# Kernel optimization log

Hardware: AMD Instinct MI355X
Metric: run time of the kernel (lower is better)

## Reference

```python
import jax, jax.numpy as jnp
import numpy as np

N = 131072          # batch of (action, condition) pairs
ACT_D = 12          # action_dim
COND_D = 256        # condition_dim
K = 256             # num_embeddings (codebook size)
E = 16              # embedding_dim
H1, H2 = 512, 256   # encoder_hidden_dims
COMMIT = 0.25       # commitment_cost
EPS_NORM = 1e-12    # F.normalize eps


def _normalize(x):
    n = jnp.linalg.norm(x, axis=-1, keepdims=True)
    return x / jnp.maximum(n, EPS_NORM)


def setup_inputs() -> dict:
    key = jax.random.key(0)
    ks = jax.random.split(key, 16)
    s = 0.02
    return {
        "actions": jax.random.normal(ks[0], (N, ACT_D), jnp.float32),
        "conditions": jax.random.normal(ks[1], (N, COND_D), jnp.float32),
        # encoder: (COND_D+ACT_D) -> H1 -> H2 -> E  (weights stored [in, out])
        "enc_w1": jax.random.normal(ks[2], (COND_D + ACT_D, H1), jnp.float32) * s,
        "enc_b1": jnp.zeros((H1,), jnp.float32),
        "enc_w2": jax.random.normal(ks[3], (H1, H2), jnp.float32) * s,
        "enc_b2": jnp.zeros((H2,), jnp.float32),
        "enc_w3": jax.random.normal(ks[4], (H2, E), jnp.float32) * s,
        "enc_b3": jnp.zeros((E,), jnp.float32),
        # decoder: (COND_D+E) -> H2 -> H1 -> ACT_D
        "dec_w1": jax.random.normal(ks[5], (COND_D + E, H2), jnp.float32) * s,
        "dec_b1": jnp.zeros((H2,), jnp.float32),
        "dec_w2": jax.random.normal(ks[6], (H2, H1), jnp.float32) * s,
        "dec_b2": jnp.zeros((H1,), jnp.float32),
        "dec_w3": jax.random.normal(ks[7], (H1, ACT_D), jnp.float32) * s,
        "dec_b3": jnp.zeros((ACT_D,), jnp.float32),
        # codebook, init U(-1/K, 1/K) like nn.Embedding in the module
        "embedding": jax.random.uniform(ks[8], (K, E), jnp.float32, -1.0 / K, 1.0 / K),
    }


def reference(actions, conditions, enc_w1, enc_b1, enc_w2, enc_b2, enc_w3, enc_b3,
              dec_w1, dec_b1, dec_w2, dec_b2, dec_w3, dec_b3, embedding):
    sg = jax.lax.stop_gradient
    elu = jax.nn.elu

    # ---- encoder ----
    x = jnp.concatenate([actions, conditions], axis=-1)          # [N, ACT_D+COND_D]
    h = elu(x @ enc_w1 + enc_b1)
    h = elu(h @ enc_w2 + enc_b2)
    z = h @ enc_w3 + enc_b3                                      # [N, E]

    # ---- vector quantizer (distance='cos') ----
    normed_in = sg(_normalize(z))                                # inputs.detach()
    normed_w = _normalize(embedding)
    distances = normed_in @ normed_w.T                           # [N, K] cosine sims

    idx = jnp.argmax(distances, axis=-1)                         # [N]
    quantized = embedding[idx]                                   # one-hot @ codebook == gather

    e_latent_loss = COMMIT * jnp.mean((sg(quantized) - z) ** 2)
    q_latent_loss = jnp.mean((quantized - sg(z)) ** 2)
    quantized_st = z + sg(quantized - z)                         # straight-through

    counts = jnp.zeros((K,), distances.dtype).at[idx].add(1.0)
    avg_probs = counts / N                                       # mean of one-hot encodings
    perplexity = jnp.exp(-jnp.sum(avg_probs * jnp.log(avg_probs + 1e-10)))

    # ---- contrastive loss (training branch, deterministic part) ----
    sortd = jnp.sort(distances, axis=0)                          # ascending per codeword
    n_pos = max(1, N // K)
    dis_pos = jnp.mean(sortd[-n_pos:, :], axis=0, keepdims=True) # [1, K] hardest positives
    dis_neg = sortd[: N // 2, :]                                 # [N//2, K]
    dis = jnp.concatenate([dis_pos, dis_neg], axis=0).T / 0.07   # [K, 1+N//2]
    # cross-entropy with target class 0
    contra_loss = jnp.mean(jax.nn.logsumexp(dis, axis=1) - dis[:, 0])

    # ---- decoder ----
    d = jnp.concatenate([quantized_st, conditions], axis=-1)     # [N, E+COND_D]
    d = elu(d @ dec_w1 + dec_b1)
    d = elu(d @ dec_w2 + dec_b2)
    reconstructed = d @ dec_w3 + dec_b3                          # [N, ACT_D]

    reconstruction_loss = jnp.mean((reconstructed - actions) ** 2)

    return (reconstructed, quantized_st, idx.astype(jnp.int32), q_latent_loss,
            e_latent_loss, contra_loss, perplexity, reconstruction_loss)
```

## Files before the change

kernel.cpp:

```cpp
#include <hip/hip_runtime.h>
#include <hip/hip_bf16.h>
#include <math.h>

#define NROWS 131072
#define ACT_D 12
#define COND_D 256
#define KEMB 256
#define EDIM 16
#define H1D 512
#define H2D 256
#define NB 16384

typedef __attribute__((ext_vector_type(8))) _Float16 half8;
typedef __attribute__((ext_vector_type(4))) float floatx4;
typedef unsigned short ushort_t;

#define LO_SCALE 4096.0f
#define INV_LO_SCALE 2.44140625e-4f


__global__ void init_kernel(int* counts, float* outScal) {
    int t = threadIdx.x;
    counts[t] = 0;
    if (t < 5) outScal[t] = 0.0f;
}

__device__ inline ushort_t f16bits(_Float16 h) { return __builtin_bit_cast(ushort_t, h); }
__device__ inline float f16pair(ushort_t a, ushort_t b) {
    return (float)__builtin_bit_cast(_Float16, a)
         + (float)__builtin_bit_cast(_Float16, b) * INV_LO_SCALE;
}
__device__ inline void splitf(float v, ushort_t& hi, ushort_t& lo) {
    _Float16 h = (_Float16)v;
    _Float16 l = (_Float16)((v - (float)h) * LO_SCALE);
    hi = f16bits(h); lo = f16bits(l);
}

__device__ inline void gload_lds16(const void* g, void* lds) {
    __builtin_amdgcn_global_load_lds((const __attribute__((address_space(1))) void*)g,
                                     (__attribute__((address_space(3))) void*)lds, 16, 0, 0);
}

__global__ __launch_bounds__(256)
void convw_kernel(const float* __restrict__ W, ushort_t* __restrict__ Whi,
                  ushort_t* __restrict__ Wlo, int K, int N, int Kp)
{
    int n = blockIdx.x;
    int k = blockIdx.y * 256 + threadIdx.x;
    if (k >= Kp) return;
    float v = (k < K) ? W[(long)k * N + n] : 0.0f;
    ushort_t h, l; splitf(v, h, l);
    Whi[(long)n * Kp + k] = h;
    Wlo[(long)n * Kp + k] = l;
}

template<int CONCAT>
__global__ __launch_bounds__(256, 3)
void gemm_f16x3_kernel(const void* A0v, const void* A1v,
                       const ushort_t* __restrict__ Bhi, const ushort_t* __restrict__ Blo,
                       const float* __restrict__ bias,
                       ushort_t* __restrict__ Chi, ushort_t* __restrict__ Clo,
                       int Nw, int Kp, int Kvalid)
{
    __shared__ uint lds[4096];
    const int tid = threadIdx.x;
    const int w = tid >> 6, l = tid & 63;
    const int quad = l >> 4, lr = l & 15;
    const long rowBase = (long)blockIdx.x * 64;
    const int colBase = blockIdx.y * 128;
    const int nQ = w * 32;

    floatx4 accH[4][2], accX[4][2];
#pragma unroll
    for (int i = 0; i < 4; ++i)
#pragma unroll
        for (int j = 0; j < 2; ++j) { accH[i][j] = (floatx4)(0.0f); accX[i][j] = (floatx4)(0.0f); }

    const long nIdx0 = colBase + nQ + lr;
    const ushort_t* pF0h = Bhi + nIdx0 * Kp + quad * 8;
    const ushort_t* pF1h = pF0h + 16 * Kp;
    const ushort_t* pF0l = Blo + nIdx0 * Kp + quad * 8;
    const ushort_t* pF1l = pF0l + 16 * Kp;

    uint4 bch0, bch1, bcl0, bcl1;
    uint4 bnh0, bnh1, bnl0, bnl1;
    auto loadBcur = [&](int k0) {
        bch0 = *(const uint4*)(pF0h + k0);
        bch1 = *(const uint4*)(pF1h + k0);
        bcl0 = *(const uint4*)(pF0l + k0);
        bcl1 = *(const uint4*)(pF1l + k0);
    };
    auto loadBnext = [&](int k0) {
        bnh0 = *(const uint4*)(pF0h + k0);
        bnh1 = *(const uint4*)(pF1h + k0);
        bnl0 = *(const uint4*)(pF0l + k0);
        bnl1 = *(const uint4*)(pF1l + k0);
    };
    auto promoteB = [&]() {
        bch0 = bnh0; bch1 = bnh1; bcl0 = bnl0; bcl1 = bnl1;
    };

    const ushort_t* pAh = (const ushort_t*)A0v + (rowBase + l) * Kp + w * 8;
    const ushort_t* pAl = (const ushort_t*)A1v + (rowBase + l) * Kp + w * 8;
    auto stageA0 = [&](int buf, int k0) {
        uint* d = &lds[buf * 2048 + w * 256];
        gload_lds16(pAh + k0, d);
        gload_lds16(pAl + k0, d + 1024);
    };

    const float* A1p = (const float*)A0v;
    const float* A2p = (const float*)A1v;
    const long grow = rowBase + l;

    auto aload = [&](float* v, int k0) {
        const int kk = k0 + w * 8;
        if (kk >= CONCAT && kk + 8 <= Kvalid) {
            const float* p = A2p + grow * COND_D + (kk - CONCAT);
            *(float4*)&v[0] = *(const float4*)p;
            *(float4*)&v[4] = *(const float4*)(p + 4);
        } else if (kk + 8 <= CONCAT) {
            const float* p = A1p + grow * CONCAT + kk;
            *(float4*)&v[0] = *(const float4*)p;
            *(float4*)&v[4] = *(const float4*)(p + 4);
        } else {
#pragma unroll
            for (int i = 0; i < 8; ++i) {
                int k = kk + i;
                v[i] = (k < CONCAT) ? A1p[grow * CONCAT + k]
                     : (k < Kvalid) ? A2p[grow * COND_D + (k - CONCAT)] : 0.0f;
            }
        }
    };
    auto awrite = [&](int buf, const float* v) {
        uint hh[4], ll[4];
#pragma unroll
        for (int i = 0; i < 4; ++i) {
            ushort_t h0, l0, h1, l1;
            splitf(v[2 * i], h0, l0);
            splitf(v[2 * i + 1], h1, l1);
            hh[i] = (uint)h0 | ((uint)h1 << 16);
            ll[i] = (uint)l0 | ((uint)l1 << 16);
        }
        *(uint4*)&lds[buf * 2048 + w * 256 + l * 4]        = *(uint4*)hh;
        *(uint4*)&lds[buf * 2048 + 1024 + w * 256 + l * 4] = *(uint4*)ll;
    };

    auto compute = [&](int buf) {
        const int base = buf * 2048;
        half8 bh0 = __builtin_bit_cast(half8, bch0);
        half8 bh1 = __builtin_bit_cast(half8, bch1);
        half8 bl0 = __builtin_bit_cast(half8, bcl0);
        half8 bl1 = __builtin_bit_cast(half8, bcl1);
#pragma unroll
        for (int im = 0; im < 4; ++im) {
            int aoff = base + quad * 256 + (im * 16 + lr) * 4;
            half8 ah = __builtin_bit_cast(half8, *(uint4*)&lds[aoff]);
            half8 al = __builtin_bit_cast(half8, *(uint4*)&lds[aoff + 1024]);
            accH[im][0] = __builtin_amdgcn_mfma_f32_16x16x32_f16(ah, bh0, accH[im][0], 0, 0, 0);
            accX[im][0] = __builtin_amdgcn_mfma_f32_16x16x32_f16(ah, bl0, accX[im][0], 0, 0, 0);
            accX[im][0] = __builtin_amdgcn_mfma_f32_16x16x32_f16(al, bh0, accX[im][0], 0, 0, 0);
            accH[im][1] = __builtin_amdgcn_mfma_f32_16x16x32_f16(ah, bh1, accH[im][1], 0, 0, 0);
            accX[im][1] = __builtin_amdgcn_mfma_f32_16x16x32_f16(ah, bl1, accX[im][1], 0, 0, 0);
            accX[im][1] = __builtin_amdgcn_mfma_f32_16x16x32_f16(al, bh1, accX[im][1], 0, 0, 0);
        }
    };

    const int kTiles = Kp / 32;
    int cur = 0;
    float v[8];

    if constexpr (CONCAT == 0) {
        stageA0(0, 0);
        loadBcur(0);
        __syncthreads();
    } else {
        aload(v, 0);
        loadBcur(0);
        awrite(0, v);
        __syncthreads();
    }

    for (int t = 0; t < kTiles; ++t) {
        const bool hasNext = (t + 1 < kTiles);
        const int k0n = (t + 1) * 32;
        if constexpr (CONCAT == 0) {
            if (hasNext) {
                stageA0(cur ^ 1, k0n);
                loadBnext(k0n);
            }
            compute(cur);
        } else {
            if (hasNext) {
                aload(v, k0n);
                loadBnext(k0n);
            }
            compute(cur);
            if (hasNext) awrite(cur ^ 1, v);
        }
        __syncthreads();
        if (hasNext) promoteB();
        cur ^= 1;
    }

    float bv[2];
#pragma unroll
    for (int jn = 0; jn < 2; ++jn) bv[jn] = bias[colBase + nQ + jn * 16 + lr];
#pragma unroll
    for (int im = 0; im < 4; ++im) {
#pragma unroll
        for (int jn = 0; jn < 2; ++jn) {
            int n = colBase + nQ + jn * 16 + lr;
#pragma unroll
            for (int rr = 0; rr < 4; ++rr) {
                long m = rowBase + im * 16 + quad * 4 + rr;
                float x = accH[im][jn][rr] + accX[im][jn][rr] * INV_LO_SCALE + bv[jn];
                x = x > 0.0f ? x : (expf(x) - 1.0f);
                ushort_t h, lo; splitf(x, h, lo);
                long idx = m * Nw + n;
                Chi[idx] = h;
                Clo[idx] = lo;
            }
        }
    }
}

__global__ __launch_bounds__(256)
void quantize_kernel(const ushort_t* __restrict__ h2hi, const ushort_t* __restrict__ h2lo,
                     const float* __restrict__ W3,
                     const float* __restrict__ b3, const float* __restrict__ emb,
                     float* __restrict__ distT, float* __restrict__ outQ,
                     float* __restrict__ outIdx, int* __restrict__ counts,
                     float* __restrict__ qsum)
{
    __shared__ float h2t[16 * 260];
    __shared__ float w3t[16 * 260];
    __shared__ float nwt[256 * 20];
    __shared__ float zt[16 * 17];
    __shared__ float dt[16 * 257];
    __shared__ int   lcnt[256];
    __shared__ float swred[4];

    int t = threadIdx.x;
    long rowBase = (long)blockIdx.x * 16;

    for (int it = 0; it < 16; ++it) {
        long idx = (rowBase + it) * 256 + t;
        h2t[it * 260 + t] = f16pair(h2hi[idx], h2lo[idx]);
    }
    for (int it = 0; it < 16; ++it) {
        int flat = it * 256 + t;
        int j = flat >> 4, c = flat & 15;
        w3t[c * 260 + j] = W3[flat];
    }
    {
        float e0[16]; float ss = 0.f;
#pragma unroll
        for (int i = 0; i < 16; ++i) { e0[i] = emb[t * 16 + i]; ss += e0[i] * e0[i]; }
        float inv = 1.0f / fmaxf(sqrtf(ss), 1e-12f);
#pragma unroll
        for (int i = 0; i < 16; ++i) nwt[t * 20 + i] = e0[i] * inv;
    }
    lcnt[t] = 0;
    __syncthreads();

    int r = t >> 4, c = t & 15;
    float zacc = b3[c];
    for (int j4 = 0; j4 < 64; ++j4) {
        float4 h = *(const float4*)&h2t[r * 260 + j4 * 4];
        float4 w = *(const float4*)&w3t[c * 260 + j4 * 4];
        zacc += h.x * w.x + h.y * w.y + h.z * w.z + h.w * w.w;
    }
    float ss = zacc * zacc;
#pragma unroll
    for (int m = 1; m < 16; m <<= 1) ss += __shfl_xor(ss, m, 64);
    zt[r * 17 + c] = zacc / fmaxf(sqrtf(ss), 1e-12f);
    __syncthreads();

    float zr[16];
#pragma unroll
    for (int e = 0; e < 16; ++e) zr[e] = zt[r * 17 + e];
    float best = -1e30f; int bidx = 0;
    for (int cc = 0; cc < 16; ++cc) {
        int col = cc * 16 + c;
        float d = 0.f;
#pragma unroll
        for (int e4 = 0; e4 < 4; ++e4) {
            float4 wv = *(const float4*)&nwt[col * 20 + e4 * 4];
            d += zr[e4 * 4 + 0] * wv.x + zr[e4 * 4 + 1] * wv.y
               + zr[e4 * 4 + 2] * wv.z + zr[e4 * 4 + 3] * wv.w;
        }
        dt[r * 257 + col] = d;
        if (d > best || (d == best && col < bidx)) { best = d; bidx = col; }
    }
#pragma unroll
    for (int m = 1; m < 16; m <<= 1) {
        float ov = __shfl_xor(best, m, 64);
        int   oi = __shfl_xor(bidx, m, 64);
        if (ov > best || (ov == best && oi < bidx)) { best = ov; bidx = oi; }
    }

    float q = emb[bidx * 16 + c];
    outQ[(rowBase + r) * 16 + c] = q;
    float df = q - zacc;
    float part = df * df;
#pragma unroll
    for (int m = 1; m < 64; m <<= 1) part += __shfl_xor(part, m, 64);
    if ((t & 63) == 0) swred[t >> 6] = part;
    if (c == 0) {
        outIdx[rowBase + r] = (float)bidx;
        atomicAdd(&lcnt[bidx], 1);
    }
    __syncthreads();
    if (t == 0) atomicAdd(qsum, swred[0] + swred[1] + swred[2] + swred[3]);
    if (lcnt[t] > 0) atomicAdd(&counts[t], lcnt[t]);

    int rr = t & 15, cg = t >> 4;
    for (int i = 0; i < 16; ++i) {
        int col = i * 16 + cg;
        distT[(long)col * NROWS + rowBase + rr] = dt[rr * 257 + col];
    }
}

__global__ __launch_bounds__(1024)
void selA_kernel(const float* __restrict__ distT, int* __restrict__ stats)
{
    __shared__ int hist[NB];
    __shared__ int part[1024];
    int t = threadIdx.x, c = blockIdx.x;
    for (int i = t; i < NB; i += 1024) hist[i] = 0;
    __syncthreads();
    const float* col = distT + (long)c * NROWS;
    for (int i = t; i < NROWS; i += 1024) {
        float v = col[i];
        int b = (int)((v + 1.0f) * (NB * 0.5f));
        b = min(max(b, 0), NB - 1);
        atomicAdd(&hist[b], 1);
    }
    __syncthreads();
    const int CH = NB / 1024;
    int s = 0;
    for (int i = 0; i < CH; ++i) s += hist[t * CH + i];
    part[t] = s;
    __syncthreads();
    if (t == 0) {
        int target = NROWS / 2;
        int cum = 0; int chunk = 0;
        while (cum + part[chunk] < target) { cum += part[chunk]; ++chunk; }
        int b = chunk * CH;
        while (cum + hist[b] < target) { cum += hist[b]; ++b; }
        int medBin = b, needLow = target - cum, cntMed = hist[b];
        int cumA = 0; chunk = 1023;
        while (cumA + part[chunk] < 512) { cumA += part[chunk]; --chunk; }
        b = chunk * CH + CH - 1;
        while (cumA + hist[b] < 512) { cumA += hist[b]; --b; }
        int topBin = b, needTop = 512 - cumA, cntTop = hist[b];
        int* st = stats + c * 6;
        st[0] = medBin; st[1] = needLow; st[2] = cntMed;
        st[3] = topBin; st[4] = needTop; st[5] = cntTop;
    }
}

__global__ __launch_bounds__(1024)
void selB_kernel(const float* __restrict__ distT, const int* __restrict__ stats,
                 float* __restrict__ contra_sum)
{
    __shared__ float red[64];
    int t = threadIdx.x, c = blockIdx.x;
    const int* st = stats + c * 6;
    int medBin = st[0], needLow = st[1], cntMed = st[2];
    int topBin = st[3], needTop = st[4], cntTop = st[5];
    const float binw = 2.0f / NB;
    float mUp = -1.0f + (medBin + 1) * binw;
    const float INVT = 1.0f / 0.07f;
    const float* col = distT + (long)c * NROWS;
    float topS = 0.f, tbS = 0.f, lowS = 0.f, mbS = 0.f;
    for (int i = t; i < NROWS; i += 1024) {
        float v = col[i];
        int b = (int)((v + 1.0f) * (NB * 0.5f));
        b = min(max(b, 0), NB - 1);
        if (b > topBin)       topS += v;
        else if (b == topBin) tbS += v;
        if (b < medBin)       lowS += expf((v - mUp) * INVT);
        else if (b == medBin) mbS  += expf((v - mUp) * INVT);
    }
#pragma unroll
    for (int m = 1; m < 64; m <<= 1) {
        topS += __shfl_xor(topS, m, 64);
        tbS  += __shfl_xor(tbS, m, 64);
        lowS += __shfl_xor(lowS, m, 64);
        mbS  += __shfl_xor(mbS, m, 64);
    }
    if ((t & 63) == 0) {
        int wv = t >> 6;
        red[wv * 4 + 0] = topS; red[wv * 4 + 1] = tbS;
        red[wv * 4 + 2] = lowS; red[wv * 4 + 3] = mbS;
    }
    __syncthreads();
    if (t == 0) {
        float T0 = 0, T1 = 0, T2 = 0, T3 = 0;
        for (int wv = 0; wv < 16; ++wv) {
            T0 += red[wv * 4 + 0]; T1 += red[wv * 4 + 1];
            T2 += red[wv * 4 + 2]; T3 += red[wv * 4 + 3];
        }
        float dis_pos = (T0 + needTop * (T1 / cntTop)) * (1.0f / 512.0f);
        float S = T2 + needLow * (T3 / cntMed);
        float colContra = log1pf(S * expf((mUp - dis_pos) * INVT));
        atomicAdd(contra_sum, colContra);
    }
}

__global__ __launch_bounds__(256)
void dec3_kernel(const ushort_t* __restrict__ d2hi, const ushort_t* __restrict__ d2lo,
                 const float* __restrict__ W,
                 const float* __restrict__ bias, const float* __restrict__ actions,
                 float* __restrict__ rec, float* __restrict__ recon_sum)
{
    __shared__ float dtile[16 * 516];
    __shared__ float wt[512 * 12];
    __shared__ float red2[4];
    int t = threadIdx.x;
    long rowBase = (long)blockIdx.x * 16;
    for (int it = 0; it < 24; ++it) wt[it * 256 + t] = W[it * 256 + t];
    for (int it = 0; it < 32; ++it) {
        int flat = it * 256 + t;
        int r = flat >> 9, k = flat & 511;
        long idx = (rowBase + r) * 512 + k;
        dtile[r * 516 + k] = f16pair(d2hi[idx], d2lo[idx]);
    }
    __syncthreads();
    float part = 0.f;
    if (t < 192) {
        int r = t / 12, cc = t % 12;
        float acc = bias[cc];
        for (int k4 = 0; k4 < 128; ++k4) {
            float4 h = *(const float4*)&dtile[r * 516 + k4 * 4];
            acc += h.x * wt[(k4 * 4 + 0) * 12 + cc] + h.y * wt[(k4 * 4 + 1) * 12 + cc]
                 + h.z * wt[(k4 * 4 + 2) * 12 + cc] + h.w * wt[(k4 * 4 + 3) * 12 + cc];
        }
        rec[(rowBase + r) * 12 + cc] = acc;
        float df = acc - actions[(rowBase + r) * 12 + cc];
        part = df * df;
    }
#pragma unroll
    for (int m = 1; m < 64; m <<= 1) part += __shfl_xor(part, m, 64);
    if ((t & 63) == 0) red2[t >> 6] = part;
    __syncthreads();
    if (t == 0) atomicAdd(recon_sum, red2[0] + red2[1] + red2[2] + red2[3]);
}

__global__ void finalize_kernel(const int* __restrict__ counts, float* __restrict__ outScal)
{
    __shared__ float red[4];
    int t = threadIdx.x;
    float p = counts[t] * (1.0f / NROWS);
    float term = p * logf(p + 1e-10f);
#pragma unroll
    for (int m = 1; m < 64; m <<= 1) term += __shfl_xor(term, m, 64);
    if ((t & 63) == 0) red[t >> 6] = term;
    __syncthreads();
    if (t == 0) {
        float hsum = red[0] + red[1] + red[2] + red[3];
        float qsum = outScal[0], contra = outScal[2], recon = outScal[4];
        float ql = qsum * (1.0f / (NROWS * 16.0f));
        outScal[0] = ql;
        outScal[1] = 0.25f * ql;
        outScal[2] = contra * (1.0f / 256.0f);
        outScal[3] = expf(-hsum);
        outScal[4] = recon * (1.0f / (NROWS * 12.0f));
    }
}

extern "C" void kernel_launch(void* const* d_in, const int* in_sizes, int n_in,
                              void* d_out, int out_size, void* d_ws, size_t ws_size,
                              hipStream_t stream)
{
    const float* actions    = (const float*)d_in[0];
    const float* conditions = (const float*)d_in[1];
    const float* enc_w1 = (const float*)d_in[2];
    const float* enc_b1 = (const float*)d_in[3];
    const float* enc_w2 = (const float*)d_in[4];
    const float* enc_b2 = (const float*)d_in[5];
    const float* enc_w3 = (const float*)d_in[6];
    const float* enc_b3 = (const float*)d_in[7];
    const float* dec_w1 = (const float*)d_in[8];
    const float* dec_b1 = (const float*)d_in[9];
    const float* dec_w2 = (const float*)d_in[10];
    const float* dec_b2 = (const float*)d_in[11];
    const float* dec_w3 = (const float*)d_in[12];
    const float* dec_b3 = (const float*)d_in[13];
    const float* emb    = (const float*)d_in[14];

    float* out     = (float*)d_out;
    float* outRec  = out;
    float* outQ    = out + (long)NROWS * 12;
    float* outIdx  = out + (long)NROWS * 28;
    float* outScal = out + (long)NROWS * 29;

    ushort_t* wb    = (ushort_t*)d_out;
    ushort_t* w1hi  = wb;            ushort_t* w1lo  = wb + 147456;
    ushort_t* w2hi  = wb + 294912;   ushort_t* w2lo  = wb + 425984;
    ushort_t* wd1hi = wb + 557056;   ushort_t* wd1lo = wb + 630784;
    ushort_t* wd2hi = wb + 704512;   ushort_t* wd2lo = wb + 835584;

    float* ws = (float*)d_ws;
    int* counts = (int*)ws;
    int* stats  = (int*)(ws + 256);
    ushort_t* h2hi = (ushort_t*)(ws + 1792);
    ushort_t* h2lo = (ushort_t*)(ws + 16779008);
    ushort_t* d1hi = h2hi;
    ushort_t* d1lo = h2lo;
    float*    P1   = ws + 33556224;
    ushort_t* h1hi = (ushort_t*)P1;
    ushort_t* h1lo = (ushort_t*)(ws + 67110656);
    float*    distT = P1;
    ushort_t* d2hi = h1hi;
    ushort_t* d2lo = h1lo;

    hipLaunchKernelGGL(init_kernel, dim3(1), dim3(256), 0, stream, counts, outScal);
    hipLaunchKernelGGL(convw_kernel, dim3(512, 2), dim3(256), 0, stream, enc_w1, w1hi, w1lo, 268, 512, 288);
    hipLaunchKernelGGL(convw_kernel, dim3(256, 2), dim3(256), 0, stream, enc_w2, w2hi, w2lo, 512, 256, 512);
    hipLaunchKernelGGL(convw_kernel, dim3(256, 2), dim3(256), 0, stream, dec_w1, wd1hi, wd1lo, 272, 256, 288);
    hipLaunchKernelGGL(convw_kernel, dim3(512, 1), dim3(256), 0, stream, dec_w2, wd2hi, wd2lo, 256, 512, 256);
    hipLaunchKernelGGL((gemm_f16x3_kernel<ACT_D>), dim3(2048, 4), dim3(256), 0, stream,
                       (const void*)actions, (const void*)conditions, w1hi, w1lo, enc_b1,
                       h1hi, h1lo, H1D, 288, 268);
    hipLaunchKernelGGL((gemm_f16x3_kernel<0>), dim3(2048, 2), dim3(256), 0, stream,
                       (const void*)h1hi, (const void*)h1lo, w2hi, w2lo, enc_b2,
                       h2hi, h2lo, H2D, 512, 512);
    hipLaunchKernelGGL(quantize_kernel, dim3(8192), dim3(256), 0, stream,
                       h2hi, h2lo, enc_w3, enc_b3, emb, distT, outQ, outIdx, counts, &outScal[0]);
    hipLaunchKernelGGL(selA_kernel, dim3(256), dim3(1024), 0, stream, distT, stats);
    hipLaunchKernelGGL(selB_kernel, dim3(256), dim3(1024), 0, stream, distT, stats, &outScal[2]);
    hipLaunchKernelGGL((gemm_f16x3_kernel<EDIM>), dim3(2048, 2), dim3(256), 0, stream,
                       (const void*)outQ, (const void*)conditions, wd1hi, wd1lo, dec_b1,
                       d1hi, d1lo, H2D, 288, 272);
    hipLaunchKernelGGL((gemm_f16x3_kernel<0>), dim3(2048, 4), dim3(256), 0, stream,
                       (const void*)d1hi, (const void*)d1lo, wd2hi, wd2lo, dec_b2,
                       d2hi, d2lo, H1D, 256, 256);
    hipLaunchKernelGGL(dec3_kernel, dim3(8192), dim3(256), 0, stream,
                       d2hi, d2lo, dec_w3, dec_b3, actions, outRec, &outScal[4]);
    hipLaunchKernelGGL(finalize_kernel, dim3(1), dim3(256), 0, stream, counts, outScal);
}
```

Baseline: 1.524 ms.

## Halve GEMM row tile to 32 and remap A staging across waves

```diff
diff --git a/kernel.cpp b/kernel.cpp
--- a/kernel.cpp
+++ b/kernel.cpp
@@ -55,107 +55,100 @@
 }
 
 template<int CONCAT>
-__global__ __launch_bounds__(256, 3)
+__global__ __launch_bounds__(256, 4)
 void gemm_f16x3_kernel(const void* A0v, const void* A1v,
                        const ushort_t* __restrict__ Bhi, const ushort_t* __restrict__ Blo,
                        const float* __restrict__ bias,
                        ushort_t* __restrict__ Chi, ushort_t* __restrict__ Clo,
                        int Nw, int Kp, int Kvalid)
 {
-    __shared__ uint lds[4096];
+    __shared__ uint lds[2048];
     const int tid = threadIdx.x;
     const int w = tid >> 6, l = tid & 63;
     const int quad = l >> 4, lr = l & 15;
-    const long rowBase = (long)blockIdx.x * 64;
+    const long rowBase = (long)blockIdx.x * 32;
     const int colBase = blockIdx.y * 128;
     const int nQ = w * 32;
 
-    floatx4 accH[4][2], accX[4][2];
-#pragma unroll
-    for (int i = 0; i < 4; ++i)
+    floatx4 accH[2][2], accX[2][2];
+#pragma unroll
+    for (int i = 0; i < 2; ++i)
 #pragma unroll
         for (int j = 0; j < 2; ++j) { accH[i][j] = (floatx4)(0.0f); accX[i][j] = (floatx4)(0.0f); }
 
-    const long nIdx0 = colBase + nQ + lr;
-    const ushort_t* pF0h = Bhi + nIdx0 * Kp + quad * 8;
-    const ushort_t* pF1h = pF0h + 16 * Kp;
-    const ushort_t* pF0l = Blo + nIdx0 * Kp + quad * 8;
-    const ushort_t* pF1l = pF0l + 16 * Kp;
+    const uint off0 = (uint)((colBase + nQ + lr) * Kp + quad * 8);
+    const uint off1 = off0 + (uint)(16 * Kp);
 
     uint4 bch0, bch1, bcl0, bcl1;
     uint4 bnh0, bnh1, bnl0, bnl1;
     auto loadBcur = [&](int k0) {
-        bch0 = *(const uint4*)(pF0h + k0);
-        bch1 = *(const uint4*)(pF1h + k0);
-        bcl0 = *(const uint4*)(pF0l + k0);
-        bcl1 = *(const uint4*)(pF1l + k0);
+        bch0 = *(const uint4*)(Bhi + off0 + k0);
+        bch1 = *(const uint4*)(Bhi + off1 + k0);
+        bcl0 = *(const uint4*)(Blo + off0 + k0);
+        bcl1 = *(const uint4*)(Blo + off1 + k0);
     };
     auto loadBnext = [&](int k0) {
-        bnh0 = *(const uint4*)(pF0h + k0);
-        bnh1 = *(const uint4*)(pF1h + k0);
-        bnl0 = *(const uint4*)(pF0l + k0);
-        bnl1 = *(const uint4*)(pF1l + k0);
+        bnh0 = *(const uint4*)(Bhi + off0 + k0);
+        bnh1 = *(const uint4*)(Bhi + off1 + k0);
+        bnl0 = *(const uint4*)(Blo + off0 + k0);
+        bnl1 = *(const uint4*)(Blo + off1 + k0);
     };
     auto promoteB = [&]() {
         bch0 = bnh0; bch1 = bnh1; bcl0 = bnl0; bcl1 = bnl1;
     };
 
-    const ushort_t* pAh = (const ushort_t*)A0v + (rowBase + l) * Kp + w * 8;
-    const ushort_t* pAl = (const ushort_t*)A1v + (rowBase + l) * Kp + w * 8;
+    const ushort_t* aSrc = (const ushort_t*)((w < 2) ? A0v : A1v);
+    const ushort_t* pAdma = aSrc + (rowBase + (l & 31)) * Kp
+                                 + ((w & 1) * 2 + (l >> 5)) * 8;
+    const int ldsWaveBase = (w >> 1) * 512 + (w & 1) * 256;
     auto stageA0 = [&](int buf, int k0) {
-        uint* d = &lds[buf * 2048 + w * 256];
-        gload_lds16(pAh + k0, d);
-        gload_lds16(pAl + k0, d + 1024);
+        gload_lds16(pAdma + k0, &lds[buf * 1024 + ldsWaveBase]);
     };
 
     const float* A1p = (const float*)A0v;
     const float* A2p = (const float*)A1v;
-    const long grow = rowBase + l;
-
-    auto aload = [&](float* v, int k0) {
-        const int kk = k0 + w * 8;
-        if (kk >= CONCAT && kk + 8 <= Kvalid) {
-            const float* p = A2p + grow * COND_D + (kk - CONCAT);
-            *(float4*)&v[0] = *(const float4*)p;
-            *(float4*)&v[4] = *(const float4*)(p + 4);
-        } else if (kk + 8 <= CONCAT) {
-            const float* p = A1p + grow * CONCAT + kk;
-            *(float4*)&v[0] = *(const float4*)p;
-            *(float4*)&v[4] = *(const float4*)(p + 4);
+    const int cr = tid >> 3, cseg = tid & 7;
+    const long crow = rowBase + cr;
+    const int cwOff = (cseg >> 1) * 128 + cr * 4 + (cseg & 1) * 2;
+
+    float v[4];
+    auto cload = [&](int k0) {
+        const int kk = k0 + cseg * 4;
+        if (kk >= CONCAT && kk + 4 <= Kvalid) {
+            *(float4*)v = *(const float4*)(A2p + crow * COND_D + (kk - CONCAT));
+        } else if (kk + 4 <= CONCAT) {
+            *(float4*)v = *(const float4*)(A1p + crow * CONCAT + kk);
         } else {
 #pragma unroll
-            for (int i = 0; i < 8; ++i) {
+            for (int i = 0; i < 4; ++i) {
                 int k = kk + i;
-                v[i] = (k < CONCAT) ? A1p[grow * CONCAT + k]
-                     : (k < Kvalid) ? A2p[grow * COND_D + (k - CONCAT)] : 0.0f;
+                v[i] = (k < CONCAT) ? A1p[crow * CONCAT + k]
+                     : (k < Kvalid) ? A2p[crow * COND_D + (k - CONCAT)] : 0.0f;
             }
         }
     };
-    auto awrite = [&](int buf, const float* v) {
-        uint hh[4], ll[4];
-#pragma unroll
-        for (int i = 0; i < 4; ++i) {
-            ushort_t h0, l0, h1, l1;
-            splitf(v[2 * i], h0, l0);
-            splitf(v[2 * i + 1], h1, l1);
-            hh[i] = (uint)h0 | ((uint)h1 << 16);
-            ll[i] = (uint)l0 | ((uint)l1 << 16);
-        }
-        *(uint4*)&lds[buf * 2048 + w * 256 + l * 4]        = *(uint4*)hh;
-        *(uint4*)&lds[buf * 2048 + 1024 + w * 256 + l * 4] = *(uint4*)ll;
+    auto cwrite = [&](int buf) {
+        ushort_t h0, l0, h1, l1, h2, l2, h3, l3;
+        splitf(v[0], h0, l0); splitf(v[1], h1, l1);
+        splitf(v[2], h2, l2); splitf(v[3], h3, l3);
+        uint2 hh, ll;
+        hh.x = (uint)h0 | ((uint)h1 << 16); hh.y = (uint)h2 | ((uint)h3 << 16);
+        ll.x = (uint)l0 | ((uint)l1 << 16); ll.y = (uint)l2 | ((uint)l3 << 16);
+        *(uint2*)&lds[buf * 1024 + cwOff]       = hh;
+        *(uint2*)&lds[buf * 1024 + 512 + cwOff] = ll;
     };
 
     auto compute = [&](int buf) {
-        const int base = buf * 2048;
+        const int base = buf * 1024;
         half8 bh0 = __builtin_bit_cast(half8, bch0);
         half8 bh1 = __builtin_bit_cast(half8, bch1);
         half8 bl0 = __builtin_bit_cast(half8, bcl0);
         half8 bl1 = __builtin_bit_cast(half8, bcl1);
 #pragma unroll
-        for (int im = 0; im < 4; ++im) {
-            int aoff = base + quad * 256 + (im * 16 + lr) * 4;
+        for (int im = 0; im < 2; ++im) {
+            int aoff = base + quad * 128 + (im * 16 + lr) * 4;
             half8 ah = __builtin_bit_cast(half8, *(uint4*)&lds[aoff]);
-            half8 al = __builtin_bit_cast(half8, *(uint4*)&lds[aoff + 1024]);
+            half8 al = __builtin_bit_cast(half8, *(uint4*)&lds[aoff + 512]);
             accH[im][0] = __builtin_amdgcn_mfma_f32_16x16x32_f16(ah, bh0, accH[im][0], 0, 0, 0);
             accX[im][0] = __builtin_amdgcn_mfma_f32_16x16x32_f16(ah, bl0, accX[im][0], 0, 0, 0);
             accX[im][0] = __builtin_amdgcn_mfma_f32_16x16x32_f16(al, bh0, accX[im][0], 0, 0, 0);
@@ -167,16 +160,15 @@
 
     const int kTiles = Kp / 32;
     int cur = 0;
-    float v[8];
 
     if constexpr (CONCAT == 0) {
         stageA0(0, 0);
         loadBcur(0);
         __syncthreads();
     } else {
-        aload(v, 0);
+        cload(0);
         loadBcur(0);
-        awrite(0, v);
+        cwrite(0);
         __syncthreads();
     }
 
@@ -191,11 +183,11 @@
             compute(cur);
         } else {
             if (hasNext) {
-                aload(v, k0n);
+                cload(k0n);
                 loadBnext(k0n);
             }
             compute(cur);
-            if (hasNext) awrite(cur ^ 1, v);
+            if (hasNext) cwrite(cur ^ 1);
         }
         __syncthreads();
         if (hasNext) promoteB();
@@ -206,7 +198,7 @@
 #pragma unroll
     for (int jn = 0; jn < 2; ++jn) bv[jn] = bias[colBase + nQ + jn * 16 + lr];
 #pragma unroll
-    for (int im = 0; im < 4; ++im) {
+    for (int im = 0; im < 2; ++im) {
 #pragma unroll
         for (int jn = 0; jn < 2; ++jn) {
             int n = colBase + nQ + jn * 16 + lr;
@@ -521,20 +513,20 @@
     hipLaunchKernelGGL(convw_kernel, dim3(256, 2), dim3(256), 0, stream, enc_w2, w2hi, w2lo, 512, 256, 512);
     hipLaunchKernelGGL(convw_kernel, dim3(256, 2), dim3(256), 0, stream, dec_w1, wd1hi, wd1lo, 272, 256, 288);
     hipLaunchKernelGGL(convw_kernel, dim3(512, 1), dim3(256), 0, stream, dec_w2, wd2hi, wd2lo, 256, 512, 256);
-    hipLaunchKernelGGL((gemm_f16x3_kernel<ACT_D>), dim3(2048, 4), dim3(256), 0, stream,
+    hipLaunchKernelGGL((gemm_f16x3_kernel<ACT_D>), dim3(4096, 4), dim3(256), 0, stream,
                        (const void*)actions, (const void*)conditions, w1hi, w1lo, enc_b1,
                        h1hi, h1lo, H1D, 288, 268);
-    hipLaunchKernelGGL((gemm_f16x3_kernel<0>), dim3(2048, 2), dim3(256), 0, stream,
+    hipLaunchKernelGGL((gemm_f16x3_kernel<0>), dim3(4096, 2), dim3(256), 0, stream,
                        (const void*)h1hi, (const void*)h1lo, w2hi, w2lo, enc_b2,
                        h2hi, h2lo, H2D, 512, 512);
     hipLaunchKernelGGL(quantize_kernel, dim3(8192), dim3(256), 0, stream,
                        h2hi, h2lo, enc_w3, enc_b3, emb, distT, outQ, outIdx, counts, &outScal[0]);
     hipLaunchKernelGGL(selA_kernel, dim3(256), dim3(1024), 0, stream, distT, stats);
     hipLaunchKernelGGL(selB_kernel, dim3(256), dim3(1024), 0, stream, distT, stats, &outScal[2]);
-    hipLaunchKernelGGL((gemm_f16x3_kernel<EDIM>), dim3(2048, 2), dim3(256), 0, stream,
+    hipLaunchKernelGGL((gemm_f16x3_kernel<EDIM>), dim3(4096, 2), dim3(256), 0, stream,
                        (const void*)outQ, (const void*)conditions, wd1hi, wd1lo, dec_b1,
                        d1hi, d1lo, H2D, 288, 272);
-    hipLaunchKernelGGL((gemm_f16x3_kernel<0>), dim3(2048, 4), dim3(256), 0, stream,
+    hipLaunchKernelGGL((gemm_f16x3_kernel<0>), dim3(4096, 4), dim3(256), 0, stream,
                        (const void*)d1hi, (const void*)d1lo, wd2hi, wd2lo, dec_b2,
                        d2hi, d2lo, H1D, 256, 256);
     hipLaunchKernelGGL(dec3_kernel, dim3(8192), dim3(256), 0, stream,
```

Result: slower. 1.790 ms (+17.5%).
